# Optimization experiments

Hardware: AMD Instinct MI355X
Metric: run time of the kernel (lower is better)

The kernel has to match this reference:

```python
import jax, jax.numpy as jnp
import numpy as np
from jax import lax

WS = 8          # window size
HEADS = 8
DIM = 192       # embed_dim == v_dim inside block
HD = DIM // HEADS
SCALE = HD ** -0.5
EPS = 1e-5


def _rel_pos_index(ws):
    coords = np.stack(np.meshgrid(np.arange(ws), np.arange(ws), indexing='ij'))  # (2,ws,ws)
    cf = coords.reshape(2, -1)                       # (2, n)
    rel = (cf[:, :, None] - cf[:, None, :]).transpose(1, 2, 0).astype(np.int64)  # (n,n,2)
    rel[..., 0] += ws - 1
    rel[..., 1] += ws - 1
    rel[..., 0] *= 2 * ws - 1
    return rel.sum(-1)                               # (n, n) int


def _ln(x, w, b):
    m = jnp.mean(x, axis=-1, keepdims=True)
    v = jnp.mean(jnp.square(x - m), axis=-1, keepdims=True)
    return (x - m) * lax.rsqrt(v + EPS) * w + b


def _conv3x3(x, w, b):
    y = lax.conv_general_dilated(x, w, (1, 1), ((1, 1), (1, 1)),
                                 dimension_numbers=('NCHW', 'OIHW', 'NCHW'))
    return y + b[None, :, None, None]


def setup_inputs():
    key = jax.random.key(0)
    ks = jax.random.split(key, 24)
    f = lambda k, shape: (jax.random.normal(k, shape, jnp.float32) * 0.02)
    inp = {
        'x': jax.random.normal(ks[0], (8, 96, 128, 128), jnp.float32),
        'v': jax.random.normal(ks[1], (8, 96, 128, 128), jnp.float32),
        'pq_w': f(ks[2], (DIM, 96, 3, 3)), 'pq_b': f(ks[3], (DIM,)),
        'pv_w': f(ks[4], (DIM, 96, 3, 3)), 'pv_b': f(ks[5], (DIM,)),
        'n1_w': jnp.ones((DIM,)), 'n1_b': jnp.zeros((DIM,)),
        'n2_w': jnp.ones((DIM,)), 'n2_b': jnp.zeros((DIM,)),
        'n3_w': jnp.ones((DIM,)), 'n3_b': jnp.zeros((DIM,)),
        'n4_w': jnp.ones((DIM,)), 'n4_b': jnp.zeros((DIM,)),
        'q_w': f(ks[6], (DIM, DIM)),
        'kv_w': f(ks[7], (2 * DIM, DIM)),
        'ap_w': f(ks[8], (DIM, DIM)), 'ap_b': f(ks[9], (DIM,)),
        'rpb': f(ks[10], ((2 * WS - 1) * (2 * WS - 1), HEADS)),
        'fc1_w': f(ks[11], (4 * DIM, DIM)), 'fc1_b': f(ks[12], (4 * DIM,)),
        'fc2_w': f(ks[13], (DIM, 4 * DIM)), 'fc2_b': f(ks[14], (DIM,)),
    }
    return inp


def reference(x, v, pq_w, pq_b, pv_w, pv_b, n1_w, n1_b, n2_w, n2_b, n3_w, n3_b,
              n4_w, n4_b, q_w, kv_w, ap_w, ap_b, rpb, fc1_w, fc1_b, fc2_w, fc2_b):
    # conv projections (input_dim != embed_dim, v_dim != embed_dim)
    x = _conv3x3(x, pq_w, pq_b)
    v = _conv3x3(v, pv_w, pv_b)
    x_proj, v_proj = x, v
    b, c, h, w = x.shape
    n = WS * WS

    xs = _ln(x.reshape(b, c, h * w).transpose(0, 2, 1), n1_w, n1_b).reshape(b, h, w, c)
    vs = _ln(v.reshape(b, c, h * w).transpose(0, 2, 1), n2_w, n2_b).reshape(b, h, w, c)

    pad_r = (WS - w % WS) % WS
    pad_b_ = (WS - h % WS) % WS
    if pad_r or pad_b_:
        xs = jnp.pad(xs, ((0, 0), (0, pad_b_), (0, pad_r), (0, 0)))
        vs = jnp.pad(vs, ((0, 0), (0, pad_b_), (0, pad_r), (0, 0)))
    hp, wp = h + pad_b_, w + pad_r

    def partition(t):  # (b,hp,wp,c) -> (nw, n, c)
        t = t.reshape(b, hp // WS, WS, wp // WS, WS, c)
        return t.transpose(0, 1, 3, 2, 4, 5).reshape(-1, n, c)

    xw = partition(xs)
    vw = partition(vs)

    # cross-window attention
    q = (xw @ q_w.T).reshape(-1, n, HEADS, HD).transpose(0, 2, 1, 3) * SCALE  # (nw,H,n,hd)
    kv = (vw @ kv_w.T).reshape(-1, n, 2, HEADS, HD).transpose(2, 0, 3, 1, 4)
    k, vv = kv[0], kv[1]                                                     # (nw,H,n,hd)
    attn = jnp.einsum('whqd,whkd->whqk', q, k)
    rel_idx = _rel_pos_index(WS)                                             # static (n,n)
    bias = rpb[rel_idx.reshape(-1)].reshape(n, n, HEADS).transpose(2, 0, 1)  # (H,n,n)
    attn = jax.nn.softmax(attn + bias[None], axis=-1)
    out = jnp.einsum('whqk,whkd->whqd', attn, vv).transpose(0, 2, 1, 3).reshape(-1, n, c)
    out = out @ ap_w.T + ap_b                                                # (nw,n,c)

    # window reverse + crop
    out = out.reshape(b, hp // WS, wp // WS, WS, WS, c).transpose(0, 1, 3, 2, 4, 5)
    out = out.reshape(b, hp, wp, c)[:, :h, :w, :].reshape(b, h * w, c)

    # mlp: note original does x = mlp(norm3(x)); x = x + drop_path(x) -> 2*mlp_out
    m = _ln(out, n3_w, n3_b)
    m = jax.nn.gelu(m @ fc1_w.T + fc1_b, approximate=False) @ fc2_w.T + fc2_b
    m = m + m
    m = _ln(m, n4_w, n4_b)
    m = m.reshape(b, h, w, c).transpose(0, 3, 1, 2)
    return m + x_proj + v_proj
```

## Files before the change

kernel.cpp:

```cpp
#include <hip/hip_runtime.h>
#include <hip/hip_bf16.h>
#include <math.h>

typedef _Float16 f16;
typedef _Float16 half8 __attribute__((ext_vector_type(8)));
typedef float f32x4 __attribute__((ext_vector_type(4)));

#define IMG 128
#define CIN 96
#define CH  192
#define SCALE_Q 0.2041241452319315f

__device__ __forceinline__ f32x4 mfma16(half8 a, half8 b, f32x4 c) {
  return __builtin_amdgcn_mfma_f32_16x16x32_f16(a, b, c, 0, 0, 0);
}

template <bool WH>
__device__ __forceinline__ half8 loadW(const void* W, int row, int k, int ldk) {
  if constexpr (WH) {
    return *(const half8*)((const f16*)W + (size_t)row * ldk + k);
  } else {
    const float* p = (const float*)W + (size_t)row * ldk + k;
    const float4 a = *(const float4*)p;
    const float4 b = *(const float4*)(p + 4);
    half8 h;
    h[0] = (f16)a.x; h[1] = (f16)a.y; h[2] = (f16)a.z; h[3] = (f16)a.w;
    h[4] = (f16)b.x; h[5] = (f16)b.y; h[6] = (f16)b.z; h[7] = (f16)b.w;
    return h;
  }
}

__device__ __forceinline__ float gelu(float x) {
  const float u = 0.70710678118654752f * x;
  const float a = fabsf(u);
  const float t = __builtin_amdgcn_rcpf(1.0f + 0.3275911f * a);
  const float poly = t * (0.254829592f + t * (-0.284496736f +
                     t * (1.421413741f + t * (-1.453152027f + t * 1.061405429f))));
  float er = 1.0f - poly * __expf(-u * u);
  er = (u < 0.f) ? -er : er;
  return 0.5f * x * (1.0f + er);
}

__global__ __launch_bounds__(256) void reorder_w(
    const float* __restrict__ pq_w, const float* __restrict__ pv_w,
    const float* __restrict__ qW, const float* __restrict__ kvW,
    f16* __restrict__ Wr, f16* __restrict__ wq16) {
  const int i = blockIdx.x * 256 + threadIdx.x;
  if (i < 2 * 192 * 864) {
    const int which = i / (192 * 864);
    const int rem = i - which * (192 * 864);
    const int co = rem / 864;
    const int kk = rem - co * 864;
    const int s = kk / 96;
    const int ci = kk - s * 96;
    const float* src = which ? pv_w : pq_w;
    Wr[i] = (f16)src[co * 864 + ci * 9 + s];
  } else if (wq16) {
    const int j = i - 2 * 192 * 864;
    if (j < 110592)
      wq16[j] = (f16)(j < 36864 ? qW[j] : kvW[j - 36864]);
  }
}

__global__ __launch_bounds__(256) void reorder_w2(
    const float* __restrict__ apW, const float* __restrict__ w1,
    const float* __restrict__ w2, f16* __restrict__ dst) {
  const int i = blockIdx.x * 256 + threadIdx.x;
  if (i >= 331776) return;
  float v;
  if (i < 36864)       v = apW[i];
  else if (i < 184320) v = w1[i - 36864];
  else                 v = w2[i - 184320];
  dst[i] = (f16)v;
}

__global__ __launch_bounds__(256, 2) void conv3x3_mfma(
    const float* __restrict__ xin, const float* __restrict__ vin,
    const f16* __restrict__ Wr,
    const float* __restrict__ pq_b, const float* __restrict__ pv_b,
    f16* __restrict__ xp, f16* __restrict__ vp) {
  int bz = blockIdx.x;
  const int which = bz >> 10; bz &= 1023;
  const int b = bz >> 7;
  const int yp = (bz >> 1) & 63;
  const int xseg = bz & 1;
  const int y0 = yp * 2;
  const int x0 = xseg * 64;
  const float* in = which ? vin : xin;
  const float* bias = which ? pv_b : pq_b;
  const f16* W = Wr + (size_t)which * 192 * 864;
  f16* out = which ? vp : xp;

  __shared__ __align__(16) f16 ST[4 * 66 * 104];
  const int tid = threadIdx.x;
  #pragma unroll
  for (int batch = 0; batch < 9; ++batch) {
    float vals[11];
    bool oks[11];
    int sts[11];
    #pragma unroll
    for (int u = 0; u < 11; ++u) {
      const int i = tid + (batch * 11 + u) * 256;
      const int r = i / 6336;
      const int rem2 = i - r * 6336;
      const int c = rem2 / 66;
      const int xx = rem2 - c * 66;
      const int gy = y0 + r - 1;
      const int gx = x0 - 1 + xx;
      oks[u] = ((unsigned)gy < IMG) && ((unsigned)gx < IMG);
      const int cgy = min(max(gy, 0), IMG - 1);
      const int cgx = min(max(gx, 0), IMG - 1);
      vals[u] = in[(((size_t)b * CIN + c) * IMG + cgy) * IMG + cgx];
      sts[u] = (r * 66 + xx) * 104 + c;
    }
    #pragma unroll
    for (int u = 0; u < 11; ++u)
      ST[sts[u]] = oks[u] ? (f16)vals[u] : (f16)0.f;
  }
  __syncthreads();

  const int lane = tid & 63;
  const int wv = tid >> 6;
  const int l15 = lane & 15;
  const int quad = lane >> 4;
  const int nb = wv * 48;

  f32x4 acc[8][3];
  #pragma unroll
  for (int mt = 0; mt < 8; ++mt)
    #pragma unroll
    for (int j = 0; j < 3; ++j) acc[mt][j] = (f32x4)0.f;

  #pragma unroll
  for (int s = 0; s < 9; ++s) {
    const int ky = s / 3, kx = s - ky * 3;
    #pragma unroll
    for (int kstep = 0; kstep < 3; ++kstep) {
      const int k = kstep * 32 + quad * 8;
      half8 a[8];
      #pragma unroll
      for (int mt = 0; mt < 8; ++mt)
        a[mt] = *(const half8*)(ST + (((mt >> 2) + ky) * 66 + (mt & 3) * 16 + l15 + kx) * 104 + k);
      #pragma unroll
      for (int j = 0; j < 3; ++j) {
        const half8 bf = *(const half8*)(W + (size_t)(nb + j * 16 + l15) * 864 + s * 96 + k);
        #pragma unroll
        for (int mt = 0; mt < 8; ++mt) acc[mt][j] = mfma16(a[mt], bf, acc[mt][j]);
      }
    }
  }
  __syncthreads();

  #pragma unroll
  for (int j = 0; j < 3; ++j) {
    const int n = nb + j * 16 + l15;
    const float bn = bias[n];
    #pragma unroll
    for (int mt = 0; mt < 8; ++mt) {
      const int lt = (mt >> 2) * 64 + (mt & 3) * 16 + quad * 4;
      #pragma unroll
      for (int reg = 0; reg < 4; ++reg)
        ST[(lt + reg) * 204 + n] = (f16)(acc[mt][j][reg] + bn);
    }
  }
  __syncthreads();

  const size_t rowbase0 = ((size_t)(b * IMG + y0) * IMG + x0) * CH;
  const size_t rowbase1 = ((size_t)(b * IMG + y0 + 1) * IMG + x0) * CH;
  #pragma unroll
  for (int it = 0; it < 12; ++it) {
    const int i = tid + it * 256;
    const int tok = i / 24, c8 = i - tok * 24;
    const half8 hval = *(const half8*)(ST + tok * 204 + c8 * 8);
    const int trow = tok >> 6, tx = tok & 63;
    f16* dst = out + (trow ? rowbase1 : rowbase0) + (size_t)tx * CH + c8 * 8;
    *(half8*)dst = hval;
  }
}

template <bool WH>
__global__ __launch_bounds__(256, 1) void ln_qkv_mfma(
    f16* __restrict__ xp, const f16* __restrict__ vp,
    const float* __restrict__ n1w, const float* __restrict__ n1b,
    const float* __restrict__ n2w, const float* __restrict__ n2b,
    const void* __restrict__ qW, const void* __restrict__ kvW,
    f16* __restrict__ qb, f16* __restrict__ kb, f16* __restrict__ vb) {
  const int tid = threadIdx.x;
  const int lane = tid & 63;
  const int wv = tid >> 6;
  const int l15 = lane & 15;
  const int quad = lane >> 4;
  const int tok0 = blockIdx.x * 32;
  __shared__ __align__(16) f16 U[32 * 588];
  f16* Ax = U;
  f16* Av = U + 6400;

  {
    const int r = tid >> 3;
    const int s = tid & 7;
    const size_t gbase = (size_t)(tok0 + r) * 192 + s * 24;
    half8 hx[3], hv[3];
    const half8* px = (const half8*)(xp + gbase);
    const half8* pv = (const half8*)(vp + gbase);
    #pragma unroll
    for (int i = 0; i < 3; ++i) { hx[i] = px[i]; hv[i] = pv[i]; }
    float xv[24], vvv[24];
    float sx = 0.f, sx2 = 0.f, sv = 0.f, sv2 = 0.f;
    #pragma unroll
    for (int i = 0; i < 24; ++i) {
      xv[i] = (float)hx[i >> 3][i & 7];
      vvv[i] = (float)hv[i >> 3][i & 7];
      sx += xv[i]; sx2 += xv[i] * xv[i];
      sv += vvv[i]; sv2 += vvv[i] * vvv[i];
    }
    half8 hr[3];
    #pragma unroll
    for (int i = 0; i < 24; ++i) hr[i >> 3][i & 7] = (f16)(xv[i] + vvv[i]);
    half8* pr = (half8*)(xp + gbase);
    #pragma unroll
    for (int i = 0; i < 3; ++i) pr[i] = hr[i];
    #pragma unroll
    for (int m = 1; m < 8; m <<= 1) {
      sx += __shfl_xor(sx, m, 64); sx2 += __shfl_xor(sx2, m, 64);
      sv += __shfl_xor(sv, m, 64); sv2 += __shfl_xor(sv2, m, 64);
    }
    const float mx = sx * (1.f / 192.f);
    const float rx = rsqrtf(sx2 * (1.f / 192.f) - mx * mx + 1e-5f);
    const float mv = sv * (1.f / 192.f);
    const float rv = rsqrtf(sv2 * (1.f / 192.f) - mv * mv + 1e-5f);
    #pragma unroll
    for (int i = 0; i < 24; ++i) {
      const int c = s * 24 + i;
      Ax[r * 200 + c] = (f16)((xv[i] - mx) * rx * n1w[c] + n1b[c]);
      Av[r * 200 + c] = (f16)((vvv[i] - mv) * rv * n2w[c] + n2b[c]);
    }
  }
  __syncthreads();

  const int nb = wv * 144;
  f32x4 acc[2][9];
  #pragma unroll
  for (int mt = 0; mt < 2; ++mt)
    #pragma unroll
    for (int j = 0; j < 9; ++j) acc[mt][j] = (f32x4)0.f;

  for (int kc = 0; kc < 6; ++kc) {
    const int k = kc * 32 + quad * 8;
    half8 wb[9];
    #pragma unroll
    for (int j = 0; j < 9; ++j) {
      const int n0 = nb + j * 16;
      if (n0 < 192) wb[j] = loadW<WH>(qW, n0 + l15, k, 192);
      else          wb[j] = loadW<WH>(kvW, n0 - 192 + l15, k, 192);
    }
    const half8 ax0 = *(const half8*)(Ax + l15 * 200 + k);
    const half8 ax1 = *(const half8*)(Ax + (16 + l15) * 200 + k);
    const half8 av0 = *(const half8*)(Av + l15 * 200 + k);
    const half8 av1 = *(const half8*)(Av + (16 + l15) * 200 + k);
    #pragma unroll
    for (int j = 0; j < 9; ++j) {
      const int n0 = nb + j * 16;
      if (n0 < 192) {
        acc[0][j] = mfma16(ax0, wb[j], acc[0][j]);
        acc[1][j] = mfma16(ax1, wb[j], acc[1][j]);
      } else {
        acc[0][j] = mfma16(av0, wb[j], acc[0][j]);
        acc[1][j] = mfma16(av1, wb[j], acc[1][j]);
      }
    }
  }
  __syncthreads();

  #pragma unroll
  for (int j = 0; j < 9; ++j) {
    const int n = nb + j * 16 + l15;
    const float scale = (n < 192) ? SCALE_Q : 1.f;
    #pragma unroll
    for (int mt = 0; mt < 2; ++mt)
      #pragma unroll
      for (int reg = 0; reg < 4; ++reg) {
        const int r = mt * 16 + quad * 4 + reg;
        U[r * 588 + n] = (f16)(acc[mt][j][reg] * scale);
      }
  }
  __syncthreads();

  const int yrow = (tok0 >> 7) & 127;
  const int bb = tok0 >> 14;
  const int x0b = tok0 & 127;
  const int wib = bb * 256 + ((yrow >> 3) << 4) + (x0b >> 3);
  const int trow = (yrow & 7) * 8;
  f16* const bufs[3] = {qb, kb, vb};
  #pragma unroll
  for (int it = 0; it < 9; ++it) {
    const int i = tid + it * 256;
    const int c24 = i % 24;
    const int g = i / 24;
    const int h = g & 7;
    const int g2 = g >> 3;
    const int wloc = g2 & 3;
    const int buf = g2 >> 2;
    const int t8 = c24 / 3, c3 = c24 - t8 * 3;
    const int r = wloc * 8 + t8;
    const half8 hval = *(const half8*)(U + r * 588 + buf * 192 + h * 24 + c3 * 8);
    f16* dst = bufs[buf] + (size_t)(wib + wloc) * 12288 + (trow + t8) * 24 + h * 1536 + c3 * 8;
    *(half8*)dst = hval;
  }
}

__global__ __launch_bounds__(64) void attn64(
    const f16* __restrict__ qb, const f16* __restrict__ kb,
    const f16* __restrict__ vb, const float* __restrict__ rpb,
    f16* __restrict__ fb) {
  const int wh = blockIdx.x;
  const int h = wh & 7;
  const int w = wh >> 3;
  const int t = threadIdx.x;
  __shared__ __align__(16) float ks[64 * 24];
  __shared__ __align__(16) float vs[64 * 24];
  __shared__ float bsh[225];
  const f16* kbase = kb + (size_t)wh * 1536;
  const f16* vbase = vb + (size_t)wh * 1536;
  for (int i = t; i < 1536; i += 64) { ks[i] = (float)kbase[i]; vs[i] = (float)vbase[i]; }
  for (int i = t; i < 225; i += 64) bsh[i] = rpb[i * 8 + h];
  float q[24];
  const f16* qrow = qb + ((size_t)wh * 64 + t) * 24;
  #pragma unroll
  for (int d = 0; d < 24; ++d) q[d] = (float)qrow[d];
  __syncthreads();
  const int qy = t >> 3, qx = t & 7;
  float s[64];
  float mx = -1e30f;
  #pragma unroll
  for (int kk = 0; kk < 64; ++kk) {
    float acc = 0.f;
    #pragma unroll
    for (int d = 0; d < 24; ++d) acc += q[d] * ks[kk * 24 + d];
    const int ky = kk >> 3, kx = kk & 7;
    acc += bsh[(qy - ky + 7) * 15 + (qx - kx + 7)];
    s[kk] = acc;
    mx = fmaxf(mx, acc);
  }
  float sum = 0.f;
  #pragma unroll
  for (int kk = 0; kk < 64; ++kk) { const float e = __expf(s[kk] - mx); s[kk] = e; sum += e; }
  const float inv = 1.0f / sum;
  float o[24];
  #pragma unroll
  for (int d = 0; d < 24; ++d) o[d] = 0.f;
  #pragma unroll
  for (int kk = 0; kk < 64; ++kk) {
    const float p = s[kk];
    #pragma unroll
    for (int d = 0; d < 24; ++d) o[d] += p * vs[kk * 24 + d];
  }
  f16* orow = fb + ((size_t)w * 64 + t) * 192 + h * 24;
  #pragma unroll
  for (int d = 0; d < 24; ++d) orow[d] = (f16)(o[d] * inv);
}

__global__ __launch_bounds__(256, 2) void ap_mlp_mfma(
    const f16* __restrict__ fb, const f16* __restrict__ apW,
    const float* __restrict__ apb,
    const float* __restrict__ n3w, const float* __restrict__ n3b,
    const f16* __restrict__ w1, const float* __restrict__ b1,
    const f16* __restrict__ w2, const float* __restrict__ b2,
    const float* __restrict__ n4w, const float* __restrict__ n4b,
    const f16* __restrict__ res, float* __restrict__ out) {
  const int tid = threadIdx.x;
  const int lane = tid & 63;
  const int wv = tid >> 6;
  const int l15 = lane & 15;
  const int quad = lane >> 4;
  const int wt0 = blockIdx.x * 32;
  __shared__ __align__(16) f16 SB[32 * 776];
  __shared__ float rs3[32], rq3[32], rs4[32], rq4[32];
  if (tid < 32) { rs3[tid] = 0.f; rq3[tid] = 0.f; rs4[tid] = 0.f; rq4[tid] = 0.f; }
  for (int i = tid; i < 32 * 24; i += 256) {
    const int r = i / 24, s = i - r * 24;
    *(half8*)(SB + r * 200 + s * 8) = *(const half8*)(fb + (size_t)(wt0 + r) * 192 + s * 8);
  }
  __syncthreads();

  const int nbp = wv * 48;
  int cc[3]; float apbv[3], w3v[3], b3v[3];
  #pragma unroll
  for (int j = 0; j < 3; ++j) {
    cc[j] = nbp + j * 16 + l15;
    apbv[j] = apb[cc[j]]; w3v[j] = n3w[cc[j]]; b3v[j] = n3b[cc[j]];
  }
  const int nb1 = wv * 192;
  float b1v[12];
  #pragma unroll
  for (int j = 0; j < 12; ++j) b1v[j] = b1[nb1 + j * 16 + l15];

  f32x4 accp[2][3];
  #pragma unroll
  for (int mt = 0; mt < 2; ++mt)
    #pragma unroll
    for (int j = 0; j < 3; ++j) accp[mt][j] = (f32x4)0.f;
  #pragma unroll
  for (int g = 0; g < 2; ++g) {
    half8 wb[3][3];
    #pragma unroll
    for (int u = 0; u < 3; ++u) {
      const int k = (g * 3 + u) * 32 + quad * 8;
      #pragma unroll
      for (int j = 0; j < 3; ++j)
        wb[u][j] = *(const half8*)(apW + (size_t)cc[j] * 192 + k);
    }
    #pragma unroll
    for (int u = 0; u < 3; ++u) {
      const int k = (g * 3 + u) * 32 + quad * 8;
      const half8 a0 = *(const half8*)(SB + l15 * 200 + k);
      const half8 a1 = *(const half8*)(SB + (16 + l15) * 200 + k);
      #pragma unroll
      for (int j = 0; j < 3; ++j) {
        accp[0][j] = mfma16(a0, wb[u][j], accp[0][j]);
        accp[1][j] = mfma16(a1, wb[u][j], accp[1][j]);
      }
    }
  }
  #pragma unroll
  for (int mt = 0; mt < 2; ++mt)
    #pragma unroll
    for (int j = 0; j < 3; ++j)
      #pragma unroll
      for (int reg = 0; reg < 4; ++reg) accp[mt][j][reg] += apbv[j];

  {
    float ssum[8], ssq[8];
    #pragma unroll
    for (int mt = 0; mt < 2; ++mt)
      #pragma unroll
      for (int reg = 0; reg < 4; ++reg) {
        const int i = mt * 4 + reg;
        const float a0 = accp[mt][0][reg], a1 = accp[mt][1][reg], a2 = accp[mt][2][reg];
        ssum[i] = a0 + a1 + a2;
        ssq[i] = a0 * a0 + a1 * a1 + a2 * a2;
      }
    #pragma unroll
    for (int mm = 1; mm < 16; mm <<= 1)
      #pragma unroll
      for (int i = 0; i < 8; ++i) {
        ssum[i] += __shfl_xor(ssum[i], mm, 64);
        ssq[i] += __shfl_xor(ssq[i], mm, 64);
      }
    if (l15 == 0) {
      #pragma unroll
      for (int mt = 0; mt < 2; ++mt)
        #pragma unroll
        for (int reg = 0; reg < 4; ++reg) {
          const int row = mt * 16 + quad * 4 + reg;
          atomicAdd(&rs3[row], ssum[mt * 4 + reg]);
          atomicAdd(&rq3[row], ssq[mt * 4 + reg]);
        }
    }
  }
  __syncthreads();
  #pragma unroll
  for (int mt = 0; mt < 2; ++mt)
    #pragma unroll
    for (int reg = 0; reg < 4; ++reg) {
      const int row = mt * 16 + quad * 4 + reg;
      const float mean = rs3[row] * (1.f / 192.f);
      const float rstd = rsqrtf(rq3[row] * (1.f / 192.f) - mean * mean + 1e-5f);
      #pragma unroll
      for (int j = 0; j < 3; ++j)
        SB[row * 200 + cc[j]] = (f16)((accp[mt][j][reg] - mean) * rstd * w3v[j] + b3v[j]);
    }
  __syncthreads();

  f32x4 acc1[2][12];
  #pragma unroll
  for (int mt = 0; mt < 2; ++mt)
    #pragma unroll
    for (int j = 0; j < 12; ++j) acc1[mt][j] = (f32x4)0.f;
  for (int kc = 0; kc < 6; ++kc) {
    const int k = kc * 32 + quad * 8;
    half8 wb[12];
    #pragma unroll
    for (int j = 0; j < 12; ++j)
      wb[j] = *(const half8*)(w1 + (size_t)(nb1 + j * 16 + l15) * 192 + k);
    const half8 a0 = *(const half8*)(SB + l15 * 200 + k);
    const half8 a1 = *(const half8*)(SB + (16 + l15) * 200 + k);
    #pragma unroll
    for (int j = 0; j < 12; ++j) {
      acc1[0][j] = mfma16(a0, wb[j], acc1[0][j]);
      acc1[1][j] = mfma16(a1, wb[j], acc1[1][j]);
    }
  }
  __syncthreads();
  #pragma unroll
  for (int j = 0; j < 12; ++j) {
    const int n = nb1 + j * 16 + l15;
    #pragma unroll
    for (int mt = 0; mt < 2; ++mt)
      #pragma unroll
      for (int reg = 0; reg < 4; ++reg) {
        const int row = mt * 16 + quad * 4 + reg;
        SB[row * 776 + n] = (f16)gelu(acc1[mt][j][reg] + b1v[j]);
      }
  }
  __syncthreads();

  const int wi = wt0 >> 6;
  const int t_base = wt0 & 63;
  const int b_img = wi >> 8;
  const int wy = (wi >> 4) & 15;
  const int wx = wi & 15;
  float rr[2][3][4];
  #pragma unroll
  for (int mt = 0; mt < 2; ++mt) {
    const int t0 = t_base + mt * 16 + quad * 4;
    const int y = wy * 8 + (t0 >> 3);
    const int xx0 = wx * 8 + (t0 & 7);
    const size_t tokbase = ((size_t)(b_img * 128 + y)) * 128 + xx0;
    #pragma unroll
    for (int j = 0; j < 3; ++j)
      #pragma unroll
      for (int reg = 0; reg < 4; ++reg)
        rr[mt][j][reg] = (float)res[(tokbase + reg) * 192 + cc[j]];
  }

  f32x4 acc2[2][3];
  #pragma unroll
  for (int mt = 0; mt < 2; ++mt)
    #pragma unroll
    for (int j = 0; j < 3; ++j) acc2[mt][j] = (f32x4)0.f;
  for (int g = 0; g < 6; ++g) {
    half8 wb[4][3];
    #pragma unroll
    for (int u = 0; u < 4; ++u) {
      const int k = (g * 4 + u) * 32 + quad * 8;
      #pragma unroll
      for (int j = 0; j < 3; ++j)
        wb[u][j] = *(const half8*)(w2 + (size_t)cc[j] * 768 + k);
    }
    #pragma unroll
    for (int u = 0; u < 4; ++u) {
      const int k = (g * 4 + u) * 32 + quad * 8;
      const half8 a0 = *(const half8*)(SB + l15 * 776 + k);
      const half8 a1 = *(const half8*)(SB + (16 + l15) * 776 + k);
      #pragma unroll
      for (int j = 0; j < 3; ++j) {
        acc2[0][j] = mfma16(a0, wb[u][j], acc2[0][j]);
        acc2[1][j] = mfma16(a1, wb[u][j], acc2[1][j]);
      }
    }
  }
  float w4[3], b4[3];
  #pragma unroll
  for (int j = 0; j < 3; ++j) {
    const float bj = b2[cc[j]];
    w4[j] = n4w[cc[j]]; b4[j] = n4b[cc[j]];
    #pragma unroll
    for (int mt = 0; mt < 2; ++mt)
      #pragma unroll
      for (int reg = 0; reg < 4; ++reg)
        acc2[mt][j][reg] = 2.f * (acc2[mt][j][reg] + bj);
  }
  float ssum[8], ssq[8];
  #pragma unroll
  for (int mt = 0; mt < 2; ++mt)
    #pragma unroll
    for (int reg = 0; reg < 4; ++reg) {
      const int i = mt * 4 + reg;
      const float a0 = acc2[mt][0][reg], a1 = acc2[mt][1][reg], a2 = acc2[mt][2][reg];
      ssum[i] = a0 + a1 + a2;
      ssq[i] = a0 * a0 + a1 * a1 + a2 * a2;
    }
  #pragma unroll
  for (int mm = 1; mm < 16; mm <<= 1)
    #pragma unroll
    for (int i = 0; i < 8; ++i) {
      ssum[i] += __shfl_xor(ssum[i], mm, 64);
      ssq[i] += __shfl_xor(ssq[i], mm, 64);
    }
  if (l15 == 0) {
    #pragma unroll
    for (int mt = 0; mt < 2; ++mt)
      #pragma unroll
      for (int reg = 0; reg < 4; ++reg) {
        const int row = mt * 16 + quad * 4 + reg;
        atomicAdd(&rs4[row], ssum[mt * 4 + reg]);
        atomicAdd(&rq4[row], ssq[mt * 4 + reg]);
      }
  }
  __syncthreads();

  #pragma unroll
  for (int mt = 0; mt < 2; ++mt) {
    const int row0 = mt * 16 + quad * 4;
    const int t0 = t_base + row0;
    const int y = wy * 8 + (t0 >> 3);
    const int x0 = wx * 8 + (t0 & 7);
    float mean[4], rstd[4];
    #pragma unroll
    for (int reg = 0; reg < 4; ++reg) {
      const int row = row0 + reg;
      mean[reg] = rs4[row] * (1.f / 192.f);
      rstd[reg] = rsqrtf(rq4[row] * (1.f / 192.f) - mean[reg] * mean[reg] + 1e-5f);
    }
    #pragma unroll
    for (int j = 0; j < 3; ++j) {
      float4 o;
      float vals[4];
      #pragma unroll
      for (int reg = 0; reg < 4; ++reg)
        vals[reg] = (acc2[mt][j][reg] - mean[reg]) * rstd[reg] * w4[j] + b4[j] + rr[mt][j][reg];
      o.x = vals[0]; o.y = vals[1]; o.z = vals[2]; o.w = vals[3];
      float* dst = out + ((size_t)(b_img * 192 + cc[j])) * 16384 + (y * 128 + x0);
      *(float4*)dst = o;
    }
  }
}

extern "C" void kernel_launch(void* const* d_in, const int* in_sizes, int n_in,
                              void* d_out, int out_size, void* d_ws, size_t ws_size,
                              hipStream_t stream) {
  (void)in_sizes; (void)n_in; (void)out_size;
  const float* x    = (const float*)d_in[0];
  const float* v    = (const float*)d_in[1];
  const float* pq_w = (const float*)d_in[2];
  const float* pq_b = (const float*)d_in[3];
  const float* pv_w = (const float*)d_in[4];
  const float* pv_b = (const float*)d_in[5];
  const float* n1w  = (const float*)d_in[6];
  const float* n1b  = (const float*)d_in[7];
  const float* n2w  = (const float*)d_in[8];
  const float* n2b  = (const float*)d_in[9];
  const float* n3w  = (const float*)d_in[10];
  const float* n3b  = (const float*)d_in[11];
  const float* n4w  = (const float*)d_in[12];
  const float* n4b  = (const float*)d_in[13];
  const float* qW   = (const float*)d_in[14];
  const float* kvW  = (const float*)d_in[15];
  const float* apW  = (const float*)d_in[16];
  const float* apb  = (const float*)d_in[17];
  const float* rpb  = (const float*)d_in[18];
  const float* w1   = (const float*)d_in[19];
  const float* b1   = (const float*)d_in[20];
  const float* w2   = (const float*)d_in[21];
  const float* b2   = (const float*)d_in[22];
  float* out = (float*)d_out;

  const size_t HE = 25165824;
  f16* xp   = (f16*)d_ws;
  f16* vp   = xp + HE;
  f16* vvb  = vp + HE;
  f16* qb   = (f16*)d_out;
  f16* kb   = qb + HE;
  f16* fb   = vp;
  f16* Wr   = vvb;
  f16* wtail = vvb + HE;
  const bool big = ws_size >= (3 * HE + 110592) * sizeof(f16);

  reorder_w<<<big ? 1728 : 1296, 256, 0, stream>>>(pq_w, pv_w, qW, kvW, Wr,
                                                   big ? wtail : (f16*)nullptr);
  conv3x3_mfma<<<2048, 256, 0, stream>>>(x, v, Wr, pq_b, pv_b, xp, vp);
  if (big)
    ln_qkv_mfma<true><<<4096, 256, 0, stream>>>(xp, vp, n1w, n1b, n2w, n2b,
                                                wtail, wtail + 36864, qb, kb, vvb);
  else
    ln_qkv_mfma<false><<<4096, 256, 0, stream>>>(xp, vp, n1w, n1b, n2w, n2b,
                                                 qW, kvW, qb, kb, vvb);
  attn64<<<16384, 64, 0, stream>>>(qb, kb, vvb, rpb, fb);
  reorder_w2<<<1296, 256, 0, stream>>>(apW, w1, w2, vvb);
  ap_mlp_mfma<<<4096, 256, 0, stream>>>(fb, vvb, apb, n3w, n3b,
                                        vvb + 36864, b1, vvb + 184320, b2,
                                        n4w, n4b, xp, out);
}
```

Before: 1.031 ms.

## Pre-convert conv inputs to fp16 NHWC and vectorize attention/projection loads

Adds a transpose kernel that converts the fp32 NCHW x and v inputs into fp16 NHWC in a scratch buffer placed in the output region. The 3x3 conv can then stage its halo tile with 16-byte channel-contiguous loads instead of scalar strided fp32 gathers. The attention kernel now loads q, k and v with half8 vector loads. The projection kernel preloads all apW fragments before the barrier so weight fetches overlap the shared-memory staging. The cost is an extra kernel launch and a full read and write pass over both inputs.

```diff
diff --git a/kernel.cpp b/kernel.cpp
--- a/kernel.cpp
+++ b/kernel.cpp
@@ -3,6 +3,7 @@
 #include <math.h>
 
 typedef _Float16 f16;
+typedef _Float16 half4 __attribute__((ext_vector_type(4)));
 typedef _Float16 half8 __attribute__((ext_vector_type(8)));
 typedef float f32x4 __attribute__((ext_vector_type(4)));
 
@@ -74,9 +75,42 @@
   dst[i] = (f16)v;
 }
 
+__global__ __launch_bounds__(256) void cvt_nhwc(
+    const float* __restrict__ xin, const float* __restrict__ vin,
+    f16* __restrict__ P) {
+  int bz = blockIdx.x;
+  const int which = bz >> 10; bz &= 1023;
+  const int b = bz >> 7;
+  const int y = bz & 127;
+  const float* in = which ? vin : xin;
+  __shared__ __align__(16) f16 T[96 * 132];
+  const int tid = threadIdx.x;
+  #pragma unroll
+  for (int it = 0; it < 12; ++it) {
+    const int i = tid + it * 256;
+    const int c = i >> 5;
+    const int xq = i & 31;
+    const float4 v4 = *(const float4*)(in + (((size_t)b * CIN + c) * IMG + y) * IMG + xq * 4);
+    half4 h;
+    h[0] = (f16)v4.x; h[1] = (f16)v4.y; h[2] = (f16)v4.z; h[3] = (f16)v4.w;
+    *(half4*)(T + c * 132 + xq * 4) = h;
+  }
+  __syncthreads();
+  f16* dst = P + (size_t)which * 12582912 + (size_t)(b * IMG + y) * IMG * CIN;
+  #pragma unroll
+  for (int it = 0; it < 6; ++it) {
+    const int i2 = tid + it * 256;
+    const int tx = i2 / 12;
+    const int c0 = (i2 - tx * 12) * 8;
+    half8 h;
+    #pragma unroll
+    for (int j = 0; j < 8; ++j) h[j] = T[(c0 + j) * 132 + tx];
+    *(half8*)(dst + (size_t)tx * CIN + c0) = h;
+  }
+}
+
 __global__ __launch_bounds__(256, 2) void conv3x3_mfma(
-    const float* __restrict__ xin, const float* __restrict__ vin,
-    const f16* __restrict__ Wr,
+    const f16* __restrict__ P, const f16* __restrict__ Wr,
     const float* __restrict__ pq_b, const float* __restrict__ pv_b,
     f16* __restrict__ xp, f16* __restrict__ vp) {
   int bz = blockIdx.x;
@@ -86,36 +120,36 @@
   const int xseg = bz & 1;
   const int y0 = yp * 2;
   const int x0 = xseg * 64;
-  const float* in = which ? vin : xin;
   const float* bias = which ? pv_b : pq_b;
   const f16* W = Wr + (size_t)which * 192 * 864;
+  const f16* Pb = P + (size_t)which * 12582912;
   f16* out = which ? vp : xp;
 
   __shared__ __align__(16) f16 ST[4 * 66 * 104];
   const int tid = threadIdx.x;
-  #pragma unroll
-  for (int batch = 0; batch < 9; ++batch) {
-    float vals[11];
-    bool oks[11];
-    int sts[11];
-    #pragma unroll
-    for (int u = 0; u < 11; ++u) {
-      const int i = tid + (batch * 11 + u) * 256;
-      const int r = i / 6336;
-      const int rem2 = i - r * 6336;
-      const int c = rem2 / 66;
-      const int xx = rem2 - c * 66;
+  {
+    half8 hbuf[13];
+    int sts[13];
+    #pragma unroll
+    for (int it = 0; it < 13; ++it) {
+      const int i0 = tid + it * 256;
+      const int i = (i0 < 3168) ? i0 : 3167;
+      const int r = i / 792;
+      const int rem = i - r * 792;
+      const int xx = rem / 12;
+      const int c8 = rem - xx * 12;
       const int gy = y0 + r - 1;
       const int gx = x0 - 1 + xx;
-      oks[u] = ((unsigned)gy < IMG) && ((unsigned)gx < IMG);
       const int cgy = min(max(gy, 0), IMG - 1);
       const int cgx = min(max(gx, 0), IMG - 1);
-      vals[u] = in[(((size_t)b * CIN + c) * IMG + cgy) * IMG + cgx];
-      sts[u] = (r * 66 + xx) * 104 + c;
-    }
-    #pragma unroll
-    for (int u = 0; u < 11; ++u)
-      ST[sts[u]] = oks[u] ? (f16)vals[u] : (f16)0.f;
+      const half8 hv = *(const half8*)(Pb + ((size_t)(b * IMG + cgy) * IMG + cgx) * CIN + c8 * 8);
+      const bool ok = ((unsigned)gy < IMG) && ((unsigned)gx < IMG);
+      hbuf[it] = ok ? hv : (half8)(f16)0.f;
+      sts[it] = (i0 < 3168) ? (r * 66 + xx) * 104 + c8 * 8 : -1;
+    }
+    #pragma unroll
+    for (int it = 0; it < 13; ++it)
+      if (sts[it] >= 0) *(half8*)(ST + sts[it]) = hbuf[it];
   }
   __syncthreads();
 
@@ -321,12 +355,27 @@
   __shared__ float bsh[225];
   const f16* kbase = kb + (size_t)wh * 1536;
   const f16* vbase = vb + (size_t)wh * 1536;
-  for (int i = t; i < 1536; i += 64) { ks[i] = (float)kbase[i]; vs[i] = (float)vbase[i]; }
+  #pragma unroll
+  for (int it = 0; it < 3; ++it) {
+    const int i = t + it * 64;
+    const half8 hk = *(const half8*)(kbase + (size_t)i * 8);
+    const half8 hv = *(const half8*)(vbase + (size_t)i * 8);
+    #pragma unroll
+    for (int e = 0; e < 8; ++e) {
+      ks[i * 8 + e] = (float)hk[e];
+      vs[i * 8 + e] = (float)hv[e];
+    }
+  }
   for (int i = t; i < 225; i += 64) bsh[i] = rpb[i * 8 + h];
   float q[24];
-  const f16* qrow = qb + ((size_t)wh * 64 + t) * 24;
-  #pragma unroll
-  for (int d = 0; d < 24; ++d) q[d] = (float)qrow[d];
+  {
+    const half8* qrow = (const half8*)(qb + ((size_t)wh * 64 + t) * 24);
+    half8 hq[3];
+    #pragma unroll
+    for (int i = 0; i < 3; ++i) hq[i] = qrow[i];
+    #pragma unroll
+    for (int d = 0; d < 24; ++d) q[d] = (float)hq[d >> 3][d & 7];
+  }
   __syncthreads();
   const int qy = t >> 3, qx = t & 7;
   float s[64];
@@ -380,7 +429,6 @@
     const int r = i / 24, s = i - r * 24;
     *(half8*)(SB + r * 200 + s * 8) = *(const half8*)(fb + (size_t)(wt0 + r) * 192 + s * 8);
   }
-  __syncthreads();
 
   const int nbp = wv * 48;
   int cc[3]; float apbv[3], w3v[3], b3v[3];
@@ -389,10 +437,19 @@
     cc[j] = nbp + j * 16 + l15;
     apbv[j] = apb[cc[j]]; w3v[j] = n3w[cc[j]]; b3v[j] = n3b[cc[j]];
   }
+  half8 wp[6][3];
+  #pragma unroll
+  for (int u6 = 0; u6 < 6; ++u6) {
+    const int k = u6 * 32 + quad * 8;
+    #pragma unroll
+    for (int j = 0; j < 3; ++j)
+      wp[u6][j] = *(const half8*)(apW + (size_t)cc[j] * 192 + k);
+  }
   const int nb1 = wv * 192;
   float b1v[12];
   #pragma unroll
   for (int j = 0; j < 12; ++j) b1v[j] = b1[nb1 + j * 16 + l15];
+  __syncthreads();
 
   f32x4 accp[2][3];
   #pragma unroll
@@ -400,25 +457,14 @@
     #pragma unroll
     for (int j = 0; j < 3; ++j) accp[mt][j] = (f32x4)0.f;
   #pragma unroll
-  for (int g = 0; g < 2; ++g) {
-    half8 wb[3][3];
-    #pragma unroll
-    for (int u = 0; u < 3; ++u) {
-      const int k = (g * 3 + u) * 32 + quad * 8;
-      #pragma unroll
-      for (int j = 0; j < 3; ++j)
-        wb[u][j] = *(const half8*)(apW + (size_t)cc[j] * 192 + k);
-    }
-    #pragma unroll
-    for (int u = 0; u < 3; ++u) {
-      const int k = (g * 3 + u) * 32 + quad * 8;
-      const half8 a0 = *(const half8*)(SB + l15 * 200 + k);
-      const half8 a1 = *(const half8*)(SB + (16 + l15) * 200 + k);
-      #pragma unroll
-      for (int j = 0; j < 3; ++j) {
-        accp[0][j] = mfma16(a0, wb[u][j], accp[0][j]);
-        accp[1][j] = mfma16(a1, wb[u][j], accp[1][j]);
-      }
+  for (int u6 = 0; u6 < 6; ++u6) {
+    const int k = u6 * 32 + quad * 8;
+    const half8 a0 = *(const half8*)(SB + l15 * 200 + k);
+    const half8 a1 = *(const half8*)(SB + (16 + l15) * 200 + k);
+    #pragma unroll
+    for (int j = 0; j < 3; ++j) {
+      accp[0][j] = mfma16(a0, wp[u6][j], accp[0][j]);
+      accp[1][j] = mfma16(a1, wp[u6][j], accp[1][j]);
     }
   }
   #pragma unroll
@@ -653,12 +699,14 @@
   f16* kb   = qb + HE;
   f16* fb   = vp;
   f16* Wr   = vvb;
+  f16* P    = qb;
   f16* wtail = vvb + HE;
   const bool big = ws_size >= (3 * HE + 110592) * sizeof(f16);
 
   reorder_w<<<big ? 1728 : 1296, 256, 0, stream>>>(pq_w, pv_w, qW, kvW, Wr,
                                                    big ? wtail : (f16*)nullptr);
-  conv3x3_mfma<<<2048, 256, 0, stream>>>(x, v, Wr, pq_b, pv_b, xp, vp);
+  cvt_nhwc<<<2048, 256, 0, stream>>>(x, v, P);
+  conv3x3_mfma<<<2048, 256, 0, stream>>>(P, Wr, pq_b, pv_b, xp, vp);
   if (big)
     ln_qkv_mfma<true><<<4096, 256, 0, stream>>>(xp, vp, n1w, n1b, n2w, n2b,
                                                 wtail, wtail + 36864, qb, kb, vvb);
```

After: 1.084 ms. 5.1% more time.

## Process full 64-token window per MLP block and vectorize attention loads

Applied to the files above, without the earlier changes.

The fused projection+MLP kernel now handles a whole 64-token window with 512 threads instead of 32 tokens with 256 threads. Eight waves are split into two row groups by four column slices, so each fc1 weight fragment is reused across four row tiles and global weight traffic per token is halved. The attention kernel also switches its K/V/Q global loads from scalar fp16 reads to 8-wide vector loads. In exchange, LDS use per block doubles, accumulator registers rise in fc1, and occupancy may fall under the 512-thread launch bound.

```diff
diff --git a/kernel.cpp b/kernel.cpp
--- a/kernel.cpp
+++ b/kernel.cpp
@@ -321,12 +321,27 @@
   __shared__ float bsh[225];
   const f16* kbase = kb + (size_t)wh * 1536;
   const f16* vbase = vb + (size_t)wh * 1536;
-  for (int i = t; i < 1536; i += 64) { ks[i] = (float)kbase[i]; vs[i] = (float)vbase[i]; }
+  #pragma unroll
+  for (int it = 0; it < 3; ++it) {
+    const int i = t + it * 64;
+    const half8 hk = *(const half8*)(kbase + (size_t)i * 8);
+    const half8 hv = *(const half8*)(vbase + (size_t)i * 8);
+    #pragma unroll
+    for (int e = 0; e < 8; ++e) {
+      ks[i * 8 + e] = (float)hk[e];
+      vs[i * 8 + e] = (float)hv[e];
+    }
+  }
   for (int i = t; i < 225; i += 64) bsh[i] = rpb[i * 8 + h];
   float q[24];
-  const f16* qrow = qb + ((size_t)wh * 64 + t) * 24;
-  #pragma unroll
-  for (int d = 0; d < 24; ++d) q[d] = (float)qrow[d];
+  {
+    const half8* qrow = (const half8*)(qb + ((size_t)wh * 64 + t) * 24);
+    half8 hq[3];
+    #pragma unroll
+    for (int i = 0; i < 3; ++i) hq[i] = qrow[i];
+    #pragma unroll
+    for (int d = 0; d < 24; ++d) q[d] = (float)hq[d >> 3][d & 7];
+  }
   __syncthreads();
   const int qy = t >> 3, qx = t & 7;
   float s[64];
@@ -359,7 +374,7 @@
   for (int d = 0; d < 24; ++d) orow[d] = (f16)(o[d] * inv);
 }
 
-__global__ __launch_bounds__(256, 2) void ap_mlp_mfma(
+__global__ __launch_bounds__(512, 2) void ap_mlp_mfma(
     const f16* __restrict__ fb, const f16* __restrict__ apW,
     const float* __restrict__ apb,
     const float* __restrict__ n3w, const float* __restrict__ n3b,
@@ -372,27 +387,38 @@
   const int wv = tid >> 6;
   const int l15 = lane & 15;
   const int quad = lane >> 4;
-  const int wt0 = blockIdx.x * 32;
-  __shared__ __align__(16) f16 SB[32 * 776];
-  __shared__ float rs3[32], rq3[32], rs4[32], rq4[32];
-  if (tid < 32) { rs3[tid] = 0.f; rq3[tid] = 0.f; rs4[tid] = 0.f; rq4[tid] = 0.f; }
-  for (int i = tid; i < 32 * 24; i += 256) {
+  const int wi = blockIdx.x;
+  const int wt0 = wi * 64;
+  __shared__ __align__(16) f16 SB[64 * 776];
+  __shared__ float rs3[64], rq3[64], rs4[64], rq4[64];
+  if (tid < 64) { rs3[tid] = 0.f; rq3[tid] = 0.f; rs4[tid] = 0.f; rq4[tid] = 0.f; }
+  for (int i = tid; i < 64 * 24; i += 512) {
     const int r = i / 24, s = i - r * 24;
     *(half8*)(SB + r * 200 + s * 8) = *(const half8*)(fb + (size_t)(wt0 + r) * 192 + s * 8);
   }
-  __syncthreads();
-
-  const int nbp = wv * 48;
+
+  const int mg = wv >> 2;
+  const int ns = wv & 3;
+  const int mrow = mg * 32;
   int cc[3]; float apbv[3], w3v[3], b3v[3];
   #pragma unroll
   for (int j = 0; j < 3; ++j) {
-    cc[j] = nbp + j * 16 + l15;
+    cc[j] = ns * 48 + j * 16 + l15;
     apbv[j] = apb[cc[j]]; w3v[j] = n3w[cc[j]]; b3v[j] = n3b[cc[j]];
   }
-  const int nb1 = wv * 192;
-  float b1v[12];
-  #pragma unroll
-  for (int j = 0; j < 12; ++j) b1v[j] = b1[nb1 + j * 16 + l15];
+  half8 wp[6][3];
+  #pragma unroll
+  for (int u6 = 0; u6 < 6; ++u6) {
+    const int k = u6 * 32 + quad * 8;
+    #pragma unroll
+    for (int j = 0; j < 3; ++j)
+      wp[u6][j] = *(const half8*)(apW + (size_t)cc[j] * 192 + k);
+  }
+  const int nb1 = wv * 96;
+  float b1v[6];
+  #pragma unroll
+  for (int j = 0; j < 6; ++j) b1v[j] = b1[nb1 + j * 16 + l15];
+  __syncthreads();
 
   f32x4 accp[2][3];
   #pragma unroll
@@ -400,25 +426,14 @@
     #pragma unroll
     for (int j = 0; j < 3; ++j) accp[mt][j] = (f32x4)0.f;
   #pragma unroll
-  for (int g = 0; g < 2; ++g) {
-    half8 wb[3][3];
-    #pragma unroll
-    for (int u = 0; u < 3; ++u) {
-      const int k = (g * 3 + u) * 32 + quad * 8;
-      #pragma unroll
-      for (int j = 0; j < 3; ++j)
-        wb[u][j] = *(const half8*)(apW + (size_t)cc[j] * 192 + k);
-    }
-    #pragma unroll
-    for (int u = 0; u < 3; ++u) {
-      const int k = (g * 3 + u) * 32 + quad * 8;
-      const half8 a0 = *(const half8*)(SB + l15 * 200 + k);
-      const half8 a1 = *(const half8*)(SB + (16 + l15) * 200 + k);
-      #pragma unroll
-      for (int j = 0; j < 3; ++j) {
-        accp[0][j] = mfma16(a0, wb[u][j], accp[0][j]);
-        accp[1][j] = mfma16(a1, wb[u][j], accp[1][j]);
-      }
+  for (int u6 = 0; u6 < 6; ++u6) {
+    const int k = u6 * 32 + quad * 8;
+    const half8 a0 = *(const half8*)(SB + (mrow + l15) * 200 + k);
+    const half8 a1 = *(const half8*)(SB + (mrow + 16 + l15) * 200 + k);
+    #pragma unroll
+    for (int j = 0; j < 3; ++j) {
+      accp[0][j] = mfma16(a0, wp[u6][j], accp[0][j]);
+      accp[1][j] = mfma16(a1, wp[u6][j], accp[1][j]);
     }
   }
   #pragma unroll
@@ -451,7 +466,7 @@
       for (int mt = 0; mt < 2; ++mt)
         #pragma unroll
         for (int reg = 0; reg < 4; ++reg) {
-          const int row = mt * 16 + quad * 4 + reg;
+          const int row = mrow + mt * 16 + quad * 4 + reg;
           atomicAdd(&rs3[row], ssum[mt * 4 + reg]);
           atomicAdd(&rq3[row], ssq[mt * 4 + reg]);
         }
@@ -462,7 +477,7 @@
   for (int mt = 0; mt < 2; ++mt)
     #pragma unroll
     for (int reg = 0; reg < 4; ++reg) {
-      const int row = mt * 16 + quad * 4 + reg;
+      const int row = mrow + mt * 16 + quad * 4 + reg;
       const float mean = rs3[row] * (1.f / 192.f);
       const float rstd = rsqrtf(rq3[row] * (1.f / 192.f) - mean * mean + 1e-5f);
       #pragma unroll
@@ -471,31 +486,32 @@
     }
   __syncthreads();
 
-  f32x4 acc1[2][12];
-  #pragma unroll
-  for (int mt = 0; mt < 2; ++mt)
-    #pragma unroll
-    for (int j = 0; j < 12; ++j) acc1[mt][j] = (f32x4)0.f;
+  f32x4 acc1[4][6];
+  #pragma unroll
+  for (int mt = 0; mt < 4; ++mt)
+    #pragma unroll
+    for (int j = 0; j < 6; ++j) acc1[mt][j] = (f32x4)0.f;
   for (int kc = 0; kc < 6; ++kc) {
     const int k = kc * 32 + quad * 8;
-    half8 wb[12];
-    #pragma unroll
-    for (int j = 0; j < 12; ++j)
+    half8 wb[6];
+    #pragma unroll
+    for (int j = 0; j < 6; ++j)
       wb[j] = *(const half8*)(w1 + (size_t)(nb1 + j * 16 + l15) * 192 + k);
-    const half8 a0 = *(const half8*)(SB + l15 * 200 + k);
-    const half8 a1 = *(const half8*)(SB + (16 + l15) * 200 + k);
-    #pragma unroll
-    for (int j = 0; j < 12; ++j) {
-      acc1[0][j] = mfma16(a0, wb[j], acc1[0][j]);
-      acc1[1][j] = mfma16(a1, wb[j], acc1[1][j]);
-    }
-  }
-  __syncthreads();
-  #pragma unroll
-  for (int j = 0; j < 12; ++j) {
+    half8 a[4];
+    #pragma unroll
+    for (int mt = 0; mt < 4; ++mt)
+      a[mt] = *(const half8*)(SB + (mt * 16 + l15) * 200 + k);
+    #pragma unroll
+    for (int j = 0; j < 6; ++j)
+      #pragma unroll
+      for (int mt = 0; mt < 4; ++mt) acc1[mt][j] = mfma16(a[mt], wb[j], acc1[mt][j]);
+  }
+  __syncthreads();
+  #pragma unroll
+  for (int j = 0; j < 6; ++j) {
     const int n = nb1 + j * 16 + l15;
     #pragma unroll
-    for (int mt = 0; mt < 2; ++mt)
+    for (int mt = 0; mt < 4; ++mt)
       #pragma unroll
       for (int reg = 0; reg < 4; ++reg) {
         const int row = mt * 16 + quad * 4 + reg;
@@ -504,15 +520,13 @@
   }
   __syncthreads();
 
-  const int wi = wt0 >> 6;
-  const int t_base = wt0 & 63;
   const int b_img = wi >> 8;
   const int wy = (wi >> 4) & 15;
   const int wx = wi & 15;
   float rr[2][3][4];
   #pragma unroll
   for (int mt = 0; mt < 2; ++mt) {
-    const int t0 = t_base + mt * 16 + quad * 4;
+    const int t0 = mrow + mt * 16 + quad * 4;
     const int y = wy * 8 + (t0 >> 3);
     const int xx0 = wx * 8 + (t0 & 7);
     const size_t tokbase = ((size_t)(b_img * 128 + y)) * 128 + xx0;
@@ -540,8 +554,8 @@
     #pragma unroll
     for (int u = 0; u < 4; ++u) {
       const int k = (g * 4 + u) * 32 + quad * 8;
-      const half8 a0 = *(const half8*)(SB + l15 * 776 + k);
-      const half8 a1 = *(const half8*)(SB + (16 + l15) * 776 + k);
+      const half8 a0 = *(const half8*)(SB + (mrow + l15) * 776 + k);
+      const half8 a1 = *(const half8*)(SB + (mrow + 16 + l15) * 776 + k);
       #pragma unroll
       for (int j = 0; j < 3; ++j) {
         acc2[0][j] = mfma16(a0, wb[u][j], acc2[0][j]);
@@ -582,7 +596,7 @@
     for (int mt = 0; mt < 2; ++mt)
       #pragma unroll
       for (int reg = 0; reg < 4; ++reg) {
-        const int row = mt * 16 + quad * 4 + reg;
+        const int row = mrow + mt * 16 + quad * 4 + reg;
         atomicAdd(&rs4[row], ssum[mt * 4 + reg]);
         atomicAdd(&rq4[row], ssq[mt * 4 + reg]);
       }
@@ -591,14 +605,13 @@
 
   #pragma unroll
   for (int mt = 0; mt < 2; ++mt) {
-    const int row0 = mt * 16 + quad * 4;
-    const int t0 = t_base + row0;
+    const int t0 = mrow + mt * 16 + quad * 4;
     const int y = wy * 8 + (t0 >> 3);
     const int x0 = wx * 8 + (t0 & 7);
     float mean[4], rstd[4];
     #pragma unroll
     for (int reg = 0; reg < 4; ++reg) {
-      const int row = row0 + reg;
+      const int row = t0 + reg;
       mean[reg] = rs4[row] * (1.f / 192.f);
       rstd[reg] = rsqrtf(rq4[row] * (1.f / 192.f) - mean[reg] * mean[reg] + 1e-5f);
     }
@@ -667,7 +680,7 @@
                                                  qW, kvW, qb, kb, vvb);
   attn64<<<16384, 64, 0, stream>>>(qb, kb, vvb, rpb, fb);
   reorder_w2<<<1296, 256, 0, stream>>>(apW, w1, w2, vvb);
-  ap_mlp_mfma<<<4096, 256, 0, stream>>>(fb, vvb, apb, n3w, n3b,
+  ap_mlp_mfma<<<2048, 512, 0, stream>>>(fb, vvb, apb, n3w, n3b,
                                         vvb + 36864, b1, vvb + 184320, b2,
                                         n4w, n4b, xp, out);
 }
```

After: 1.115 ms. 8.1% more time.

## Split MLP hidden dimension into two halves to shrink shared memory and raise occupancy

Applied to the files above, without the earlier changes.

The fused attention-projection and MLP kernel now processes the 768-wide hidden layer in two 384-wide halves. It computes fc1+GELU for one half into a smaller shared buffer, accumulates the matching fc2 partial sum, then repeats for the second half. This cuts shared memory and per-wave accumulator registers so launch bounds can ask for 3 blocks per CU instead of 2. The projection weights are also preloaded before the first barrier. In exchange it adds barriers and serialises the two halves.

```diff
diff --git a/kernel.cpp b/kernel.cpp
--- a/kernel.cpp
+++ b/kernel.cpp
@@ -359,7 +359,7 @@
   for (int d = 0; d < 24; ++d) orow[d] = (f16)(o[d] * inv);
 }
 
-__global__ __launch_bounds__(256, 2) void ap_mlp_mfma(
+__global__ __launch_bounds__(256, 3) void ap_mlp_mfma(
     const f16* __restrict__ fb, const f16* __restrict__ apW,
     const float* __restrict__ apb,
     const float* __restrict__ n3w, const float* __restrict__ n3b,
@@ -373,14 +373,14 @@
   const int l15 = lane & 15;
   const int quad = lane >> 4;
   const int wt0 = blockIdx.x * 32;
-  __shared__ __align__(16) f16 SB[32 * 776];
+  __shared__ __align__(16) f16 As[32 * 200];
+  __shared__ __align__(16) f16 Hh[32 * 392];
   __shared__ float rs3[32], rq3[32], rs4[32], rq4[32];
   if (tid < 32) { rs3[tid] = 0.f; rq3[tid] = 0.f; rs4[tid] = 0.f; rq4[tid] = 0.f; }
   for (int i = tid; i < 32 * 24; i += 256) {
     const int r = i / 24, s = i - r * 24;
-    *(half8*)(SB + r * 200 + s * 8) = *(const half8*)(fb + (size_t)(wt0 + r) * 192 + s * 8);
-  }
-  __syncthreads();
+    *(half8*)(As + r * 200 + s * 8) = *(const half8*)(fb + (size_t)(wt0 + r) * 192 + s * 8);
+  }
 
   const int nbp = wv * 48;
   int cc[3]; float apbv[3], w3v[3], b3v[3];
@@ -389,10 +389,22 @@
     cc[j] = nbp + j * 16 + l15;
     apbv[j] = apb[cc[j]]; w3v[j] = n3w[cc[j]]; b3v[j] = n3b[cc[j]];
   }
-  const int nb1 = wv * 192;
-  float b1v[12];
-  #pragma unroll
-  for (int j = 0; j < 12; ++j) b1v[j] = b1[nb1 + j * 16 + l15];
+  half8 wp[6][3];
+  #pragma unroll
+  for (int u6 = 0; u6 < 6; ++u6) {
+    const int k = u6 * 32 + quad * 8;
+    #pragma unroll
+    for (int j = 0; j < 3; ++j)
+      wp[u6][j] = *(const half8*)(apW + (size_t)cc[j] * 192 + k);
+  }
+  const int nh = wv * 96;
+  float b1vA[6], b1vB[6];
+  #pragma unroll
+  for (int j = 0; j < 6; ++j) {
+    b1vA[j] = b1[nh + j * 16 + l15];
+    b1vB[j] = b1[384 + nh + j * 16 + l15];
+  }
+  __syncthreads();
 
   f32x4 accp[2][3];
   #pragma unroll
@@ -400,25 +412,14 @@
     #pragma unroll
     for (int j = 0; j < 3; ++j) accp[mt][j] = (f32x4)0.f;
   #pragma unroll
-  for (int g = 0; g < 2; ++g) {
-    half8 wb[3][3];
-    #pragma unroll
-    for (int u = 0; u < 3; ++u) {
-      const int k = (g * 3 + u) * 32 + quad * 8;
-      #pragma unroll
-      for (int j = 0; j < 3; ++j)
-        wb[u][j] = *(const half8*)(apW + (size_t)cc[j] * 192 + k);
-    }
-    #pragma unroll
-    for (int u = 0; u < 3; ++u) {
-      const int k = (g * 3 + u) * 32 + quad * 8;
-      const half8 a0 = *(const half8*)(SB + l15 * 200 + k);
-      const half8 a1 = *(const half8*)(SB + (16 + l15) * 200 + k);
-      #pragma unroll
-      for (int j = 0; j < 3; ++j) {
-        accp[0][j] = mfma16(a0, wb[u][j], accp[0][j]);
-        accp[1][j] = mfma16(a1, wb[u][j], accp[1][j]);
-      }
+  for (int u6 = 0; u6 < 6; ++u6) {
+    const int k = u6 * 32 + quad * 8;
+    const half8 a0 = *(const half8*)(As + l15 * 200 + k);
+    const half8 a1 = *(const half8*)(As + (16 + l15) * 200 + k);
+    #pragma unroll
+    for (int j = 0; j < 3; ++j) {
+      accp[0][j] = mfma16(a0, wp[u6][j], accp[0][j]);
+      accp[1][j] = mfma16(a1, wp[u6][j], accp[1][j]);
     }
   }
   #pragma unroll
@@ -467,39 +468,97 @@
       const float rstd = rsqrtf(rq3[row] * (1.f / 192.f) - mean * mean + 1e-5f);
       #pragma unroll
       for (int j = 0; j < 3; ++j)
-        SB[row * 200 + cc[j]] = (f16)((accp[mt][j][reg] - mean) * rstd * w3v[j] + b3v[j]);
-    }
-  __syncthreads();
-
-  f32x4 acc1[2][12];
+        As[row * 200 + cc[j]] = (f16)((accp[mt][j][reg] - mean) * rstd * w3v[j] + b3v[j]);
+    }
+  __syncthreads();
+
+  f32x4 acc1[2][6];
   #pragma unroll
   for (int mt = 0; mt < 2; ++mt)
     #pragma unroll
-    for (int j = 0; j < 12; ++j) acc1[mt][j] = (f32x4)0.f;
+    for (int j = 0; j < 6; ++j) acc1[mt][j] = (f32x4)0.f;
   for (int kc = 0; kc < 6; ++kc) {
     const int k = kc * 32 + quad * 8;
-    half8 wb[12];
-    #pragma unroll
-    for (int j = 0; j < 12; ++j)
-      wb[j] = *(const half8*)(w1 + (size_t)(nb1 + j * 16 + l15) * 192 + k);
-    const half8 a0 = *(const half8*)(SB + l15 * 200 + k);
-    const half8 a1 = *(const half8*)(SB + (16 + l15) * 200 + k);
-    #pragma unroll
-    for (int j = 0; j < 12; ++j) {
+    half8 wb[6];
+    #pragma unroll
+    for (int j = 0; j < 6; ++j)
+      wb[j] = *(const half8*)(w1 + (size_t)(nh + j * 16 + l15) * 192 + k);
+    const half8 a0 = *(const half8*)(As + l15 * 200 + k);
+    const half8 a1 = *(const half8*)(As + (16 + l15) * 200 + k);
+    #pragma unroll
+    for (int j = 0; j < 6; ++j) {
       acc1[0][j] = mfma16(a0, wb[j], acc1[0][j]);
       acc1[1][j] = mfma16(a1, wb[j], acc1[1][j]);
     }
   }
-  __syncthreads();
-  #pragma unroll
-  for (int j = 0; j < 12; ++j) {
-    const int n = nb1 + j * 16 + l15;
+  #pragma unroll
+  for (int j = 0; j < 6; ++j) {
+    const int n = nh + j * 16 + l15;
     #pragma unroll
     for (int mt = 0; mt < 2; ++mt)
       #pragma unroll
       for (int reg = 0; reg < 4; ++reg) {
         const int row = mt * 16 + quad * 4 + reg;
-        SB[row * 776 + n] = (f16)gelu(acc1[mt][j][reg] + b1v[j]);
+        Hh[row * 392 + n] = (f16)gelu(acc1[mt][j][reg] + b1vA[j]);
+      }
+  }
+  __syncthreads();
+
+  f32x4 acc2[2][3];
+  #pragma unroll
+  for (int mt = 0; mt < 2; ++mt)
+    #pragma unroll
+    for (int j = 0; j < 3; ++j) acc2[mt][j] = (f32x4)0.f;
+  for (int g = 0; g < 3; ++g) {
+    half8 wb2[4][3];
+    #pragma unroll
+    for (int u = 0; u < 4; ++u) {
+      const int k = (g * 4 + u) * 32 + quad * 8;
+      #pragma unroll
+      for (int j = 0; j < 3; ++j)
+        wb2[u][j] = *(const half8*)(w2 + (size_t)cc[j] * 768 + k);
+    }
+    #pragma unroll
+    for (int u = 0; u < 4; ++u) {
+      const int k = (g * 4 + u) * 32 + quad * 8;
+      const half8 a0 = *(const half8*)(Hh + l15 * 392 + k);
+      const half8 a1 = *(const half8*)(Hh + (16 + l15) * 392 + k);
+      #pragma unroll
+      for (int j = 0; j < 3; ++j) {
+        acc2[0][j] = mfma16(a0, wb2[u][j], acc2[0][j]);
+        acc2[1][j] = mfma16(a1, wb2[u][j], acc2[1][j]);
+      }
+    }
+  }
+
+  #pragma unroll
+  for (int mt = 0; mt < 2; ++mt)
+    #pragma unroll
+    for (int j = 0; j < 6; ++j) acc1[mt][j] = (f32x4)0.f;
+  for (int kc = 0; kc < 6; ++kc) {
+    const int k = kc * 32 + quad * 8;
+    half8 wb[6];
+    #pragma unroll
+    for (int j = 0; j < 6; ++j)
+      wb[j] = *(const half8*)(w1 + (size_t)(384 + nh + j * 16 + l15) * 192 + k);
+    const half8 a0 = *(const half8*)(As + l15 * 200 + k);
+    const half8 a1 = *(const half8*)(As + (16 + l15) * 200 + k);
+    #pragma unroll
+    for (int j = 0; j < 6; ++j) {
+      acc1[0][j] = mfma16(a0, wb[j], acc1[0][j]);
+      acc1[1][j] = mfma16(a1, wb[j], acc1[1][j]);
+    }
+  }
+  __syncthreads();
+  #pragma unroll
+  for (int j = 0; j < 6; ++j) {
+    const int n = nh + j * 16 + l15;
+    #pragma unroll
+    for (int mt = 0; mt < 2; ++mt)
+      #pragma unroll
+      for (int reg = 0; reg < 4; ++reg) {
+        const int row = mt * 16 + quad * 4 + reg;
+        Hh[row * 392 + n] = (f16)gelu(acc1[mt][j][reg] + b1vB[j]);
       }
   }
   __syncthreads();
@@ -523,29 +582,24 @@
         rr[mt][j][reg] = (float)res[(tokbase + reg) * 192 + cc[j]];
   }
 
-  f32x4 acc2[2][3];
-  #pragma unroll
-  for (int mt = 0; mt < 2; ++mt)
-    #pragma unroll
-    for (int j = 0; j < 3; ++j) acc2[mt][j] = (f32x4)0.f;
-  for (int g = 0; g < 6; ++g) {
-    half8 wb[4][3];
+  for (int g = 3; g < 6; ++g) {
+    half8 wb2[4][3];
     #pragma unroll
     for (int u = 0; u < 4; ++u) {
       const int k = (g * 4 + u) * 32 + quad * 8;
       #pragma unroll
       for (int j = 0; j < 3; ++j)
-        wb[u][j] = *(const half8*)(w2 + (size_t)cc[j] * 768 + k);
+        wb2[u][j] = *(const half8*)(w2 + (size_t)cc[j] * 768 + k);
     }
     #pragma unroll
     for (int u = 0; u < 4; ++u) {
-      const int k = (g * 4 + u) * 32 + quad * 8;
-      const half8 a0 = *(const half8*)(SB + l15 * 776 + k);
-      const half8 a1 = *(const half8*)(SB + (16 + l15) * 776 + k);
+      const int kl = (g * 4 + u) * 32 + quad * 8 - 384;
+      const half8 a0 = *(const half8*)(Hh + l15 * 392 + kl);
+      const half8 a1 = *(const half8*)(Hh + (16 + l15) * 392 + kl);
       #pragma unroll
       for (int j = 0; j < 3; ++j) {
-        acc2[0][j] = mfma16(a0, wb[u][j], acc2[0][j]);
-        acc2[1][j] = mfma16(a1, wb[u][j], acc2[1][j]);
+        acc2[0][j] = mfma16(a0, wb2[u][j], acc2[0][j]);
+        acc2[1][j] = mfma16(a1, wb2[u][j], acc2[1][j]);
       }
     }
   }
```

New measurement: 1.031 ms. About the same (-0.1%).
